# Optimization experiments

Hardware: AMD Instinct MI355X
Metric: run time of the kernel (lower is better)

## Reference

```python
import jax, jax.numpy as jnp
import numpy as np

N = 20000
E = 640000
D = 128      # node_dim
R = 32       # rbf_dim
H = 128      # radial_hidden_dim
CUTOFF = 5.0
RES_SCALE_INIT = 0.1
LN_EPS = 1e-5


def _init_linear(key, fan_in, fan_out):
    kw, kb = jax.random.split(key)
    bound = 1.0 / np.sqrt(fan_in)
    w = jax.random.uniform(kw, (fan_in, fan_out), minval=-bound, maxval=bound, dtype=jnp.float32)
    b = jax.random.uniform(kb, (fan_out,), minval=-bound, maxval=bound, dtype=jnp.float32)
    return w, b


def setup_inputs() -> dict:
    key = jax.random.key(0)
    ks = jax.random.split(key, 16)
    x = jax.random.normal(ks[0], (N, D), dtype=jnp.float32)
    edge_src = jax.random.randint(ks[1], (E,), 0, N)
    edge_dst = jax.random.randint(ks[2], (E,), 0, N)
    edge_sh = jax.random.normal(ks[3], (E, 16), dtype=jnp.float32)
    edge_rbf = jax.random.uniform(ks[4], (E, R), dtype=jnp.float32)
    edge_len = jax.random.uniform(ks[5], (E,), dtype=jnp.float32) * 8.0  # some edges beyond cutoff

    wm_w1, wm_b1 = _init_linear(ks[6], R, H)
    wm_w2, wm_b2 = _init_linear(ks[7], H, H)
    wm_w3, wm_b3 = _init_linear(ks[8], H, D)
    eg_w1, eg_b1 = _init_linear(ks[9], R, H)
    eg_w2, eg_b2 = _init_linear(ks[10], H, 1)
    mm_w1, mm_b1 = _init_linear(ks[11], D, H)
    mm_w2, mm_b2 = _init_linear(ks[12], H, D)
    sl_w, sl_b = _init_linear(ks[13], D, D)
    ul_w, ul_b = _init_linear(ks[14], D, D)

    return {
        "x": x, "edge_src": edge_src, "edge_dst": edge_dst,
        "edge_sh": edge_sh, "edge_rbf": edge_rbf, "edge_len": edge_len,
        "ln_g": jnp.ones((D,), jnp.float32), "ln_b": jnp.zeros((D,), jnp.float32),
        "wm_w1": wm_w1, "wm_b1": wm_b1, "wm_w2": wm_w2, "wm_b2": wm_b2,
        "wm_w3": wm_w3, "wm_b3": wm_b3,
        "eg_w1": eg_w1, "eg_b1": eg_b1, "eg_w2": eg_w2, "eg_b2": eg_b2,
        "mm_w1": mm_w1, "mm_b1": mm_b1, "mm_w2": mm_w2, "mm_b2": mm_b2,
        "sl_w": sl_w, "sl_b": sl_b, "ul_w": ul_w, "ul_b": ul_b,
        "res_scale": jnp.float32(RES_SCALE_INIT),
    }


def reference(x, edge_src, edge_dst, edge_sh, edge_rbf, edge_len,
              ln_g, ln_b,
              wm_w1, wm_b1, wm_w2, wm_b2, wm_w3, wm_b3,
              eg_w1, eg_b1, eg_w2, eg_b2,
              mm_w1, mm_b1, mm_w2, mm_b2,
              sl_w, sl_b, ul_w, ul_b, res_scale):
    # pre-LayerNorm
    mu = jnp.mean(x, axis=-1, keepdims=True)
    var = jnp.var(x, axis=-1, keepdims=True)
    x_norm = (x - mu) * jax.lax.rsqrt(var + LN_EPS) * ln_g + ln_b  # [N, D]

    # cosine cutoff * sigmoid edge gate -> [E, 1]
    r = edge_len / CUTOFF
    cut = 0.5 * (jnp.cos(jnp.pi * r) + 1.0) * (edge_len <= CUTOFF).astype(x.dtype)
    g = jax.nn.silu(edge_rbf @ eg_w1 + eg_b1)
    gate = jax.nn.sigmoid(g @ eg_w2 + eg_b2)  # [E, 1]
    edge_w = cut[:, None] * gate               # [E, 1]

    # radial weight MLP [E, D]
    h = jax.nn.silu(edge_rbf @ wm_w1 + wm_b1)
    h = jax.nn.silu(h @ wm_w2 + wm_b2)
    w_rad = h @ wm_w3 + wm_b3

    # gather, gate, scatter-add
    m = x_norm[edge_src] * w_rad * edge_w       # [E, D]
    agg = jax.ops.segment_sum(m, edge_dst, num_segments=N)          # [N, D]
    norm = jax.ops.segment_sum(edge_w, edge_dst, num_segments=N)    # [N, 1]
    agg = agg / jnp.maximum(norm, 1e-8)

    # message MLP + update
    a = jax.nn.silu(agg @ mm_w1 + mm_b1)
    agg2 = a @ mm_w2 + mm_b2
    out = (x_norm @ sl_w + sl_b) + (agg2 @ ul_w + ul_b)
    return x + res_scale * out
```

## Files before the change

kernel.cpp:

```cpp
#include <hip/hip_runtime.h>
#include <math.h>

#define N_NODES 20000
#define N_EDGES 640000
#define DD 128
#define RR 32
#define HH 128
#define PI_F 3.14159265358979323846f

#define NPACK 416
#define NLN   5000
#define NHIST 2500

typedef short bf16x8 __attribute__((ext_vector_type(8)));
typedef float f32x4 __attribute__((ext_vector_type(4)));
typedef __bf16 bf16x2_t __attribute__((ext_vector_type(2)));

__device__ __forceinline__ float silu_f(float x) {
    return x * __builtin_amdgcn_rcpf(1.0f + __expf(-x));
}
__device__ __forceinline__ float sigmoid_f(float x) {
    return __builtin_amdgcn_rcpf(1.0f + __expf(-x));
}
__device__ __forceinline__ unsigned short f2bf(float x) {
// ... 52 lines not shown
    } else if (blk < NPACK + NLN) {
        int wid = ((blk - NPACK) * 256 + threadIdx.x) >> 6;
        int lane = threadIdx.x & 63;
        if (wid >= N_NODES) return;
        const float* row = x + (size_t)wid * DD;
        float v0 = row[lane], v1 = row[lane + 64];
        float s = v0 + v1, sq = v0 * v0 + v1 * v1;
        #pragma unroll
        for (int o = 32; o > 0; o >>= 1) { s += __shfl_xor(s, o); sq += __shfl_xor(sq, o); }
        float mu = s * (1.0f / 128.0f);
        float var = sq * (1.0f / 128.0f) - mu * mu;
        float inv = rsqrtf(var + 1e-5f);
        float* orow = xn + (size_t)wid * DD;
        orow[lane]      = (v0 - mu) * inv * g[lane]      + b[lane];
        orow[lane + 64] = (v1 - mu) * inv * g[lane + 64] + b[lane + 64];
    } else {
        int e = (blk - NPACK - NLN) * 256 + threadIdx.x;
        if (e < N_EDGES && elen[e] <= 5.0f) atomicAdd(&cnt[edst[e]], 1);
    }
}

__global__ __launch_bounds__(1024) void scan_kernel(const int* __restrict__ cnt,
                                                    int* __restrict__ offs,
                                                    int* __restrict__ cursor) {
    __shared__ int part[1024];
    const int t = threadIdx.x;
    const int per = 20;
    const int base = t * per;
    int s = 0;
    for (int i = 0; i < per; ++i) {
        int idx = base + i;
        if (idx < N_NODES) s += cnt[idx];
    }
    part[t] = s;
    __syncthreads();
    for (int off = 1; off < 1024; off <<= 1) {
        int v = (t >= off) ? part[t - off] : 0;
        __syncthreads();
        part[t] += v;
        __syncthreads();
    }
    int run = part[t] - s;
    for (int i = 0; i < per; ++i) {
        int idx = base + i;
        if (idx < N_NODES) {
            offs[idx] = run;
            cursor[idx] = run;
            run += cnt[idx];
        }
    }
    if (t == 1023) offs[N_NODES] = part[1023];
}

__global__ __launch_bounds__(256) void fill_kernel(const int* __restrict__ edst,
                                                   const float* __restrict__ elen,
                                                   int* __restrict__ cursor,
                                                   int* __restrict__ perm) {
    int e = blockIdx.x * 256 + threadIdx.x;
    if (e >= N_EDGES) return;
    if (elen[e] <= 5.0f) {
        int pos = atomicAdd(&cursor[edst[e]], 1);
        perm[pos] = e;
    }
}

__global__ __launch_bounds__(256, 4) void edge_seg_kernel(
    const float* __restrict__ xn,
    const int* __restrict__ esrc, const int* __restrict__ edst,
    const float* __restrict__ rbf, const float* __restrict__ elen,
    const int* __restrict__ perm, const int* __restrict__ nlive_p,
    const unsigned short* __restrict__ wp_eg1, const unsigned short* __restrict__ wp_w1,
    const unsigned short* __restrict__ wp_w2,  const unsigned short* __restrict__ wp_w3,
    const float* __restrict__ eg_b1, const float* __restrict__ eg_w2,
    const float* __restrict__ eg_b2,
    const float* __restrict__ wm_b1, const float* __restrict__ wm_b2,
    const float* __restrict__ wm_b3,
    float* __restrict__ agg, float* __restrict__ nrm)
{
    __shared__ unsigned short act[4][32 * 136];
    __shared__ float ew_s[128];
    __shared__ int   dst_s[128];

    const int nlive = nlive_p[0];
    if (blockIdx.x * 128 >= nlive) return;

    const int tid  = threadIdx.x;
    const int w    = tid >> 6;
    const int lane = tid & 63;
    const int er   = lane & 15;
    const int kq   = lane >> 4;

    const int g0 = blockIdx.x * 128 + w * 32 + er;
    const int g1 = g0 + 16;
    const bool v0 = g0 < nlive, v1 = g1 < nlive;
    const int e0 = perm[v0 ? g0 : nlive - 1];
    const int e1 = perm[v1 ? g1 : nlive - 1];

    const float4* rp = (const float4*)(rbf + (size_t)e0 * RR + kq * 8);
    bf16x8 bfr0 = frag8(rp[0], rp[1]);
    const float4* rq = (const float4*)(rbf + (size_t)e1 * RR + kq * 8);
    bf16x8 bfr1 = frag8(rq[0], rq[1]);

    const int src0 = esrc[e0], dst0 = edst[e0];
    const int src1 = esrc[e1], dst1 = edst[e1];
    const float len0 = elen[e0], len1 = elen[e1];
    const float cut0 = v0 ? 0.5f * (__cosf(PI_F * len0 * 0.2f) + 1.0f) : 0.0f;
    const float cut1 = v1 ? 0.5f * (__cosf(PI_F * len1 * 0.2f) + 1.0f) : 0.0f;

    unsigned short* buf = &act[w][0];

    float pd0 = 0.0f, pd1 = 0.0f;
    #pragma unroll
    for (int t = 0; t < 8; ++t) {
        bf16x8 ag = *(const bf16x8*)(wp_eg1 + ((size_t)t * 64 + lane) * 8);
        bf16x8 a1 = *(const bf16x8*)(wp_w1  + ((size_t)t * 64 + lane) * 8);
        f32x4 z = {0.f, 0.f, 0.f, 0.f};
        f32x4 cg0 = __builtin_amdgcn_mfma_f32_16x16x32_bf16(ag, bfr0, z, 0, 0, 0);
        f32x4 cg1 = __builtin_amdgcn_mfma_f32_16x16x32_bf16(ag, bfr1, z, 0, 0, 0);
        f32x4 c10 = __builtin_amdgcn_mfma_f32_16x16x32_bf16(a1, bfr0, z, 0, 0, 0);
        f32x4 c11 = __builtin_amdgcn_mfma_f32_16x16x32_bf16(a1, bfr1, z, 0, 0, 0);
        float4 gb = *(const float4*)(eg_b1 + t * 16 + kq * 4);
        float4 w2 = *(const float4*)(eg_w2 + t * 16 + kq * 4);
        pd0 += silu_f(cg0[0]+gb.x)*w2.x + silu_f(cg0[1]+gb.y)*w2.y
             + silu_f(cg0[2]+gb.z)*w2.z + silu_f(cg0[3]+gb.w)*w2.w;
        pd1 += silu_f(cg1[0]+gb.x)*w2.x + silu_f(cg1[1]+gb.y)*w2.y
             + silu_f(cg1[2]+gb.z)*w2.z + silu_f(cg1[3]+gb.w)*w2.w;
        float4 b1 = *(const float4*)(wm_b1 + t * 16 + kq * 4);
        *(uint2*)(buf + er * 136 + t * 16 + kq * 4) =
            make_uint2(pk2(silu_f(c10[0]+b1.x), silu_f(c10[1]+b1.y)),
                       pk2(silu_f(c10[2]+b1.z), silu_f(c10[3]+b1.w)));
        *(uint2*)(buf + (16 + er) * 136 + t * 16 + kq * 4) =
            make_uint2(pk2(silu_f(c11[0]+b1.x), silu_f(c11[1]+b1.y)),
                       pk2(silu_f(c11[2]+b1.z), silu_f(c11[3]+b1.w)));
    }
    pd0 += __shfl_xor(pd0, 16); pd0 += __shfl_xor(pd0, 32);
    pd1 += __shfl_xor(pd1, 16); pd1 += __shfl_xor(pd1, 32);
    const float eb2 = eg_b2[0];
    const float ew0 = cut0 * sigmoid_f(pd0 + eb2);
    const float ew1 = cut1 * sigmoid_f(pd1 + eb2);
    if (lane < 16) {
        ew_s[w * 32 + er] = ew0;       dst_s[w * 32 + er] = dst0;
        ew_s[w * 32 + 16 + er] = ew1;  dst_s[w * 32 + 16 + er] = dst1;
    }

    bf16x8 h0[4], h1[4];
    #pragma unroll
    for (int s = 0; s < 4; ++s) {
        h0[s] = *(const bf16x8*)(buf + er * 136 + s * 32 + kq * 8);
        h1[s] = *(const bf16x8*)(buf + (16 + er) * 136 + s * 32 + kq * 8);
    }
    #pragma unroll
    for (int t = 0; t < 8; ++t) {
        f32x4 c0 = {0.f, 0.f, 0.f, 0.f};
        f32x4 c1 = {0.f, 0.f, 0.f, 0.f};
        #pragma unroll
        for (int s = 0; s < 4; ++s) {
            bf16x8 af = *(const bf16x8*)(wp_w2 + (((size_t)s * 8 + t) * 64 + lane) * 8);
            c0 = __builtin_amdgcn_mfma_f32_16x16x32_bf16(af, h0[s], c0, 0, 0, 0);
            c1 = __builtin_amdgcn_mfma_f32_16x16x32_bf16(af, h1[s], c1, 0, 0, 0);
        }
        float4 b2 = *(const float4*)(wm_b2 + t * 16 + kq * 4);
        *(uint2*)(buf + er * 136 + t * 16 + kq * 4) =
            make_uint2(pk2(silu_f(c0[0]+b2.x), silu_f(c0[1]+b2.y)),
                       pk2(silu_f(c0[2]+b2.z), silu_f(c0[3]+b2.w)));
        *(uint2*)(buf + (16 + er) * 136 + t * 16 + kq * 4) =
            make_uint2(pk2(silu_f(c1[0]+b2.x), silu_f(c1[1]+b2.y)),
                       pk2(silu_f(c1[2]+b2.z), silu_f(c1[3]+b2.w)));
    }

    #pragma unroll
    for (int s = 0; s < 4; ++s) {
        h0[s] = *(const bf16x8*)(buf + er * 136 + s * 32 + kq * 8);
        h1[s] = *(const bf16x8*)(buf + (16 + er) * 136 + s * 32 + kq * 8);
    }
    const float* xr0 = xn + (size_t)src0 * DD;
    const float* xr1 = xn + (size_t)src1 * DD;
    #pragma unroll
    for (int t = 0; t < 8; ++t) {
        f32x4 c0 = {0.f, 0.f, 0.f, 0.f};
        f32x4 c1 = {0.f, 0.f, 0.f, 0.f};
        #pragma unroll
        for (int s = 0; s < 4; ++s) {
            bf16x8 af = *(const bf16x8*)(wp_w3 + (((size_t)s * 8 + t) * 64 + lane) * 8);
            c0 = __builtin_amdgcn_mfma_f32_16x16x32_bf16(af, h0[s], c0, 0, 0, 0);
            c1 = __builtin_amdgcn_mfma_f32_16x16x32_bf16(af, h1[s], c1, 0, 0, 0);
        }
        float4 b3 = *(const float4*)(wm_b3 + t * 16 + kq * 4);
        float4 xv0 = *(const float4*)(xr0 + t * 16 + kq * 4);
        float4 xv1 = *(const float4*)(xr1 + t * 16 + kq * 4);
        *(uint2*)(buf + er * 136 + t * 16 + kq * 4) =
            make_uint2(pk2((c0[0]+b3.x)*xv0.x*ew0, (c0[1]+b3.y)*xv0.y*ew0),
                       pk2((c0[2]+b3.z)*xv0.z*ew0, (c0[3]+b3.w)*xv0.w*ew0));
        *(uint2*)(buf + (16 + er) * 136 + t * 16 + kq * 4) =
            make_uint2(pk2((c1[0]+b3.x)*xv1.x*ew1, (c1[1]+b3.y)*xv1.y*ew1),
                       pk2((c1[2]+b3.z)*xv1.z*ew1, (c1[3]+b3.w)*xv1.w*ew1));
    }

    {
        const int rb = w * 32;
        float run0 = 0.0f, run1 = 0.0f, ewrun = 0.0f;
        int cur = dst_s[rb];
        #pragma unroll 8
        for (int i = 0; i < 32; ++i) {
            const int d = dst_s[rb + i];
            if (d != cur) {
                atomicAdd(&agg[(size_t)cur * DD + 2 * lane], run0);
                atomicAdd(&agg[(size_t)cur * DD + 2 * lane + 1], run1);
                if (lane == 0) atomicAdd(&nrm[cur], ewrun);
                run0 = 0.0f; run1 = 0.0f; ewrun = 0.0f; cur = d;
            }
            unsigned pv = *(const unsigned*)(buf + i * 136 + 2 * lane);
            run0 += __uint_as_float(pv << 16);
            run1 += __uint_as_float(pv & 0xffff0000u);
            ewrun += ew_s[rb + i];
        }
        atomicAdd(&agg[(size_t)cur * DD + 2 * lane], run0);
        atomicAdd(&agg[(size_t)cur * DD + 2 * lane + 1], run1);
        if (lane == 0) atomicAdd(&nrm[cur], ewrun);
    }
}

__global__ __launch_bounds__(256) void node_kernel(
    const float* __restrict__ x, const float* __restrict__ xn,
    const float* __restrict__ agg, const float* __restrict__ nrm,
    const unsigned short* __restrict__ wp_mm1, const unsigned short* __restrict__ wp_mm2,
    const unsigned short* __restrict__ wp_sl,  const unsigned short* __restrict__ wp_ul,
    const float* __restrict__ mm_b1, const float* __restrict__ mm_b2,
    const float* __restrict__ sl_b, const float* __restrict__ ul_b,
    const float* __restrict__ res_scale, float* __restrict__ out)
{
    __shared__ unsigned short act[4][16 * 136];

    const int tid  = threadIdx.x;
    const int w    = tid >> 6;
    const int lane = tid & 63;
    const int er   = lane & 15;
    const int kq   = lane >> 4;

    const int n  = blockIdx.x * 64 + w * 16 + er;
    const bool valid = n < N_NODES;
    const int nc = valid ? n : N_NODES - 1;

    const float rs = __builtin_amdgcn_rcpf(fmaxf(nrm[nc], 1e-8f));
    const float rscl = res_scale[0];

    bf16x8 ba[4];
    #pragma unroll
    for (int s = 0; s < 4; ++s) {
        const float4* ap = (const float4*)(agg + (size_t)nc * DD + s * 32 + kq * 8);
        float4 a = ap[0], b = ap[1];
        a.x *= rs; a.y *= rs; a.z *= rs; a.w *= rs;
        b.x *= rs; b.y *= rs; b.z *= rs; b.w *= rs;
        ba[s] = frag8(a, b);
    }

    unsigned short* buf = &act[w][0];

    #pragma unroll
    for (int t = 0; t < 8; ++t) {
        f32x4 c = {0.f, 0.f, 0.f, 0.f};
        #pragma unroll
        for (int s = 0; s < 4; ++s) {
            bf16x8 af = *(const bf16x8*)(wp_mm1 + (((size_t)s * 8 + t) * 64 + lane) * 8);
            c = __builtin_amdgcn_mfma_f32_16x16x32_bf16(af, ba[s], c, 0, 0, 0);
        }
        float4 b1 = *(const float4*)(mm_b1 + t * 16 + kq * 4);
        *(uint2*)(buf + er * 136 + t * 16 + kq * 4) =
            make_uint2(pk2(silu_f(c[0]+b1.x), silu_f(c[1]+b1.y)),
                       pk2(silu_f(c[2]+b1.z), silu_f(c[3]+b1.w)));
    }

    bf16x8 bh[4];
    #pragma unroll
    for (int s = 0; s < 4; ++s)
        bh[s] = *(const bf16x8*)(buf + er * 136 + s * 32 + kq * 8);
    #pragma unroll
    for (int t = 0; t < 8; ++t) {
        f32x4 c = {0.f, 0.f, 0.f, 0.f};
        #pragma unroll
        for (int s = 0; s < 4; ++s) {
            bf16x8 af = *(const bf16x8*)(wp_mm2 + (((size_t)s * 8 + t) * 64 + lane) * 8);
            c = __builtin_amdgcn_mfma_f32_16x16x32_bf16(af, bh[s], c, 0, 0, 0);
        }
        float4 b2 = *(const float4*)(mm_b2 + t * 16 + kq * 4);
        *(uint2*)(buf + er * 136 + t * 16 + kq * 4) =
            make_uint2(pk2(c[0]+b2.x, c[1]+b2.y), pk2(c[2]+b2.z, c[3]+b2.w));
    }

    bf16x8 bg[4], bx[4];
    #pragma unroll
    for (int s = 0; s < 4; ++s) {
        bg[s] = *(const bf16x8*)(buf + er * 136 + s * 32 + kq * 8);
        const float4* xp = (const float4*)(xn + (size_t)nc * DD + s * 32 + kq * 8);
        bx[s] = frag8(xp[0], xp[1]);
    }

    #pragma unroll
    for (int t = 0; t < 8; ++t) {
        f32x4 c = {0.f, 0.f, 0.f, 0.f};
        #pragma unroll
        for (int s = 0; s < 4; ++s) {
            bf16x8 af = *(const bf16x8*)(wp_sl + (((size_t)s * 8 + t) * 64 + lane) * 8);
            c = __builtin_amdgcn_mfma_f32_16x16x32_bf16(af, bx[s], c, 0, 0, 0);
        }
        #pragma unroll
        for (int s = 0; s < 4; ++s) {
            bf16x8 af = *(const bf16x8*)(wp_ul + (((size_t)s * 8 + t) * 64 + lane) * 8);
            c = __builtin_amdgcn_mfma_f32_16x16x32_bf16(af, bg[s], c, 0, 0, 0);
        }
        if (valid) {
            float4 sb = *(const float4*)(sl_b + t * 16 + kq * 4);
            float4 ub = *(const float4*)(ul_b + t * 16 + kq * 4);
            float4 xv = *(const float4*)(x + (size_t)n * DD + t * 16 + kq * 4);
            float4 o;
            o.x = xv.x + rscl * (c[0] + sb.x + ub.x);
            o.y = xv.y + rscl * (c[1] + sb.y + ub.y);
            o.z = xv.z + rscl * (c[2] + sb.z + ub.z);
            o.w = xv.w + rscl * (c[3] + sb.w + ub.w);
            *(float4*)(out + (size_t)n * DD + t * 16 + kq * 4) = o;
        }
    }
}

extern "C" void kernel_launch(void* const* d_in, const int* in_sizes, int n_in,
                              void* d_out, int out_size, void* d_ws, size_t ws_size,
                              hipStream_t stream) {
    const float* x     = (const float*)d_in[0];
    const int*   esrc  = (const int*)d_in[1];
    const int*   edst  = (const int*)d_in[2];
    const float* rbf   = (const float*)d_in[4];
    const float* elen  = (const float*)d_in[5];
    const float* ln_g  = (const float*)d_in[6];
    const float* ln_b  = (const float*)d_in[7];
    const float* wm_w1 = (const float*)d_in[8];
    const float* wm_b1 = (const float*)d_in[9];
    const float* wm_w2 = (const float*)d_in[10];
    const float* wm_b2 = (const float*)d_in[11];
    const float* wm_w3 = (const float*)d_in[12];
    const float* wm_b3 = (const float*)d_in[13];
    const float* eg_w1 = (const float*)d_in[14];
    const float* eg_b1 = (const float*)d_in[15];
    const float* eg_w2 = (const float*)d_in[16];
    const float* eg_b2 = (const float*)d_in[17];
    const float* mm_w1 = (const float*)d_in[18];
    const float* mm_b1 = (const float*)d_in[19];
    const float* mm_w2 = (const float*)d_in[20];
    const float* mm_b2 = (const float*)d_in[21];
    const float* sl_w  = (const float*)d_in[22];
    const float* sl_b  = (const float*)d_in[23];
    const float* ul_w  = (const float*)d_in[24];
    const float* ul_b  = (const float*)d_in[25];
    const float* rscl  = (const float*)d_in[26];

    float* xn  = (float*)d_ws;
    float* agg = xn + (size_t)N_NODES * DD;
    float* nrm = agg + (size_t)N_NODES * DD;
    int*   cnt = (int*)(nrm + N_NODES);
    unsigned short* wp = (unsigned short*)(cnt + N_NODES);
    unsigned short* wp_eg1 = wp;
    unsigned short* wp_w1  = wp_eg1 + 4096;
    unsigned short* wp_w2  = wp_w1 + 4096;
    unsigned short* wp_w3  = wp_w2 + 16384;
    unsigned short* wp_mm1 = wp_w3 + 16384;
    unsigned short* wp_mm2 = wp_mm1 + 16384;
    unsigned short* wp_sl  = wp_mm2 + 16384;
    unsigned short* wp_ul  = wp_sl + 16384;
    int* offs   = (int*)(wp_ul + 16384);
    int* cursor = offs + N_NODES + 1;
    int* perm   = cursor + N_NODES;

    hipMemsetAsync(agg, 0, (size_t)(N_NODES * DD + 2 * N_NODES) * sizeof(float), stream);
    prep_kernel<<<NPACK + NLN + NHIST, 256, 0, stream>>>(
        eg_w1, wm_w1, wm_w2, wm_w3, mm_w1, mm_w2, sl_w, ul_w, wp,
        x, ln_g, ln_b, xn, edst, elen, cnt);
    scan_kernel<<<1, 1024, 0, stream>>>(cnt, offs, cursor);
    fill_kernel<<<N_EDGES / 256, 256, 0, stream>>>(edst, elen, cursor, perm);
    edge_seg_kernel<<<N_EDGES / 128, 256, 0, stream>>>(xn, esrc, edst, rbf, elen,
        perm, offs + N_NODES,
        wp_eg1, wp_w1, wp_w2, wp_w3,
        eg_b1, eg_w2, eg_b2, wm_b1, wm_b2, wm_b3, agg, nrm);
    node_kernel<<<(N_NODES + 63) / 64, 256, 0, stream>>>(x, xn, agg, nrm,
        wp_mm1, wp_mm2, wp_sl, wp_ul,
        mm_b1, mm_b2, sl_b, ul_b, rscl, (float*)d_out);
}
```

Baseline: 243.0 us.

## Process more edges and nodes per wave to reuse MFMA weight fragments

The edge kernel now handles 64 edges per wave (four 16-edge groups) instead of 32, so each weight fragment loaded from global memory feeds four MFMAs rather than two. Next-step weight fragments are prefetched into registers to overlap their loads with compute. The node kernel likewise processes 32 nodes per wave instead of 16. The cost is higher register and LDS use, so occupancy drops (launch bounds relaxed to 2 blocks per CU), and there are half as many blocks.

```diff
diff --git a/kernel.cpp b/kernel.cpp
--- a/kernel.cpp
+++ b/kernel.cpp
@@ -140,7 +140,7 @@
     }
 }
 
-__global__ __launch_bounds__(256, 4) void edge_seg_kernel(
+__global__ __launch_bounds__(256, 2) void edge_seg_kernel(
     const float* __restrict__ xn,
     const int* __restrict__ esrc, const int* __restrict__ edst,
     const float* __restrict__ rbf, const float* __restrict__ elen,
@@ -153,12 +153,12 @@
     const float* __restrict__ wm_b3,
     float* __restrict__ agg, float* __restrict__ nrm)
 {
-    __shared__ unsigned short act[4][32 * 136];
-    __shared__ float ew_s[128];
-    __shared__ int   dst_s[128];
+    __shared__ unsigned short act[4][64 * 136];
+    __shared__ float ew_s[256];
+    __shared__ int   dst_s[256];
 
     const int nlive = nlive_p[0];
-    if (blockIdx.x * 128 >= nlive) return;
+    if (blockIdx.x * 256 >= nlive) return;
 
     const int tid  = threadIdx.x;
     const int w    = tid >> 6;
@@ -166,118 +166,151 @@
     const int er   = lane & 15;
     const int kq   = lane >> 4;
 
-    const int g0 = blockIdx.x * 128 + w * 32 + er;
-    const int g1 = g0 + 16;
-    const bool v0 = g0 < nlive, v1 = g1 < nlive;
-    const int e0 = perm[v0 ? g0 : nlive - 1];
-    const int e1 = perm[v1 ? g1 : nlive - 1];
-
-    const float4* rp = (const float4*)(rbf + (size_t)e0 * RR + kq * 8);
-    bf16x8 bfr0 = frag8(rp[0], rp[1]);
-    const float4* rq = (const float4*)(rbf + (size_t)e1 * RR + kq * 8);
-    bf16x8 bfr1 = frag8(rq[0], rq[1]);
-
-    const int src0 = esrc[e0], dst0 = edst[e0];
-    const int src1 = esrc[e1], dst1 = edst[e1];
-    const float len0 = elen[e0], len1 = elen[e1];
-    const float cut0 = v0 ? 0.5f * (__cosf(PI_F * len0 * 0.2f) + 1.0f) : 0.0f;
-    const float cut1 = v1 ? 0.5f * (__cosf(PI_F * len1 * 0.2f) + 1.0f) : 0.0f;
+    const int gbase = blockIdx.x * 256 + w * 64 + er;
+    int eidx[4]; bool val[4];
+    #pragma unroll
+    for (int g = 0; g < 4; ++g) {
+        int gi = gbase + g * 16;
+        val[g] = gi < nlive;
+        eidx[g] = perm[val[g] ? gi : nlive - 1];
+    }
+
+    bf16x8 bfr[4];
+    int srcv[4];
+    float ew[4];
+    {
+        float cut[4]; int dstv[4];
+        #pragma unroll
+        for (int g = 0; g < 4; ++g) {
+            const float4* rp = (const float4*)(rbf + (size_t)eidx[g] * RR + kq * 8);
+            bfr[g] = frag8(rp[0], rp[1]);
+            srcv[g] = esrc[eidx[g]];
+            dstv[g] = edst[eidx[g]];
+            float len = elen[eidx[g]];
+            cut[g] = val[g] ? 0.5f * (__cosf(PI_F * len * 0.2f) + 1.0f) : 0.0f;
+        }
+
+        unsigned short* buf = &act[w][0];
+
+        float pd[4] = {0.f, 0.f, 0.f, 0.f};
+        bf16x8 agc = *(const bf16x8*)(wp_eg1 + (size_t)lane * 8);
+        bf16x8 a1c = *(const bf16x8*)(wp_w1  + (size_t)lane * 8);
+        #pragma unroll
+        for (int t = 0; t < 8; ++t) {
+            const int tn = (t + 1) & 7;
+            bf16x8 agn = *(const bf16x8*)(wp_eg1 + ((size_t)tn * 64 + lane) * 8);
+            bf16x8 a1n = *(const bf16x8*)(wp_w1  + ((size_t)tn * 64 + lane) * 8);
+            const f32x4 z = {0.f, 0.f, 0.f, 0.f};
+            float4 gb = *(const float4*)(eg_b1 + t * 16 + kq * 4);
+            float4 w2 = *(const float4*)(eg_w2 + t * 16 + kq * 4);
+            float4 b1 = *(const float4*)(wm_b1 + t * 16 + kq * 4);
+            #pragma unroll
+            for (int g = 0; g < 4; ++g) {
+                f32x4 cg = __builtin_amdgcn_mfma_f32_16x16x32_bf16(agc, bfr[g], z, 0, 0, 0);
+                f32x4 c1 = __builtin_amdgcn_mfma_f32_16x16x32_bf16(a1c, bfr[g], z, 0, 0, 0);
+                pd[g] += silu_f(cg[0]+gb.x)*w2.x + silu_f(cg[1]+gb.y)*w2.y
+                       + silu_f(cg[2]+gb.z)*w2.z + silu_f(cg[3]+gb.w)*w2.w;
+                *(uint2*)(buf + (g * 16 + er) * 136 + t * 16 + kq * 4) =
+                    make_uint2(pk2(silu_f(c1[0]+b1.x), silu_f(c1[1]+b1.y)),
+                               pk2(silu_f(c1[2]+b1.z), silu_f(c1[3]+b1.w)));
+            }
+            agc = agn; a1c = a1n;
+        }
+        const float eb2 = eg_b2[0];
+        #pragma unroll
+        for (int g = 0; g < 4; ++g) {
+            pd[g] += __shfl_xor(pd[g], 16);
+            pd[g] += __shfl_xor(pd[g], 32);
+            ew[g] = cut[g] * sigmoid_f(pd[g] + eb2);
+        }
+        if (lane < 16) {
+            #pragma unroll
+            for (int g = 0; g < 4; ++g) {
+                ew_s[w * 64 + g * 16 + er] = ew[g];
+                dst_s[w * 64 + g * 16 + er] = dstv[g];
+            }
+        }
+    }
 
     unsigned short* buf = &act[w][0];
 
-    float pd0 = 0.0f, pd1 = 0.0f;
-    #pragma unroll
-    for (int t = 0; t < 8; ++t) {
-        bf16x8 ag = *(const bf16x8*)(wp_eg1 + ((size_t)t * 64 + lane) * 8);
-        bf16x8 a1 = *(const bf16x8*)(wp_w1  + ((size_t)t * 64 + lane) * 8);
-        f32x4 z = {0.f, 0.f, 0.f, 0.f};
-        f32x4 cg0 = __builtin_amdgcn_mfma_f32_16x16x32_bf16(ag, bfr0, z, 0, 0, 0);
-        f32x4 cg1 = __builtin_amdgcn_mfma_f32_16x16x32_bf16(ag, bfr1, z, 0, 0, 0);
-        f32x4 c10 = __builtin_amdgcn_mfma_f32_16x16x32_bf16(a1, bfr0, z, 0, 0, 0);
-        f32x4 c11 = __builtin_amdgcn_mfma_f32_16x16x32_bf16(a1, bfr1, z, 0, 0, 0);
-        float4 gb = *(const float4*)(eg_b1 + t * 16 + kq * 4);
-        float4 w2 = *(const float4*)(eg_w2 + t * 16 + kq * 4);
-        pd0 += silu_f(cg0[0]+gb.x)*w2.x + silu_f(cg0[1]+gb.y)*w2.y
-             + silu_f(cg0[2]+gb.z)*w2.z + silu_f(cg0[3]+gb.w)*w2.w;
-        pd1 += silu_f(cg1[0]+gb.x)*w2.x + silu_f(cg1[1]+gb.y)*w2.y
-             + silu_f(cg1[2]+gb.z)*w2.z + silu_f(cg1[3]+gb.w)*w2.w;
-        float4 b1 = *(const float4*)(wm_b1 + t * 16 + kq * 4);
-        *(uint2*)(buf + er * 136 + t * 16 + kq * 4) =
-            make_uint2(pk2(silu_f(c10[0]+b1.x), silu_f(c10[1]+b1.y)),
-                       pk2(silu_f(c10[2]+b1.z), silu_f(c10[3]+b1.w)));
-        *(uint2*)(buf + (16 + er) * 136 + t * 16 + kq * 4) =
-            make_uint2(pk2(silu_f(c11[0]+b1.x), silu_f(c11[1]+b1.y)),
-                       pk2(silu_f(c11[2]+b1.z), silu_f(c11[3]+b1.w)));
-    }
-    pd0 += __shfl_xor(pd0, 16); pd0 += __shfl_xor(pd0, 32);
-    pd1 += __shfl_xor(pd1, 16); pd1 += __shfl_xor(pd1, 32);
-    const float eb2 = eg_b2[0];
-    const float ew0 = cut0 * sigmoid_f(pd0 + eb2);
-    const float ew1 = cut1 * sigmoid_f(pd1 + eb2);
-    if (lane < 16) {
-        ew_s[w * 32 + er] = ew0;       dst_s[w * 32 + er] = dst0;
-        ew_s[w * 32 + 16 + er] = ew1;  dst_s[w * 32 + 16 + er] = dst1;
-    }
-
-    bf16x8 h0[4], h1[4];
-    #pragma unroll
-    for (int s = 0; s < 4; ++s) {
-        h0[s] = *(const bf16x8*)(buf + er * 136 + s * 32 + kq * 8);
-        h1[s] = *(const bf16x8*)(buf + (16 + er) * 136 + s * 32 + kq * 8);
-    }
-    #pragma unroll
-    for (int t = 0; t < 8; ++t) {
-        f32x4 c0 = {0.f, 0.f, 0.f, 0.f};
-        f32x4 c1 = {0.f, 0.f, 0.f, 0.f};
-        #pragma unroll
-        for (int s = 0; s < 4; ++s) {
-            bf16x8 af = *(const bf16x8*)(wp_w2 + (((size_t)s * 8 + t) * 64 + lane) * 8);
-            c0 = __builtin_amdgcn_mfma_f32_16x16x32_bf16(af, h0[s], c0, 0, 0, 0);
-            c1 = __builtin_amdgcn_mfma_f32_16x16x32_bf16(af, h1[s], c1, 0, 0, 0);
-        }
-        float4 b2 = *(const float4*)(wm_b2 + t * 16 + kq * 4);
-        *(uint2*)(buf + er * 136 + t * 16 + kq * 4) =
-            make_uint2(pk2(silu_f(c0[0]+b2.x), silu_f(c0[1]+b2.y)),
-                       pk2(silu_f(c0[2]+b2.z), silu_f(c0[3]+b2.w)));
-        *(uint2*)(buf + (16 + er) * 136 + t * 16 + kq * 4) =
-            make_uint2(pk2(silu_f(c1[0]+b2.x), silu_f(c1[1]+b2.y)),
-                       pk2(silu_f(c1[2]+b2.z), silu_f(c1[3]+b2.w)));
-    }
-
-    #pragma unroll
-    for (int s = 0; s < 4; ++s) {
-        h0[s] = *(const bf16x8*)(buf + er * 136 + s * 32 + kq * 8);
-        h1[s] = *(const bf16x8*)(buf + (16 + er) * 136 + s * 32 + kq * 8);
-    }
-    const float* xr0 = xn + (size_t)src0 * DD;
-    const float* xr1 = xn + (size_t)src1 * DD;
-    #pragma unroll
-    for (int t = 0; t < 8; ++t) {
-        f32x4 c0 = {0.f, 0.f, 0.f, 0.f};
-        f32x4 c1 = {0.f, 0.f, 0.f, 0.f};
-        #pragma unroll
-        for (int s = 0; s < 4; ++s) {
-            bf16x8 af = *(const bf16x8*)(wp_w3 + (((size_t)s * 8 + t) * 64 + lane) * 8);
-            c0 = __builtin_amdgcn_mfma_f32_16x16x32_bf16(af, h0[s], c0, 0, 0, 0);
-            c1 = __builtin_amdgcn_mfma_f32_16x16x32_bf16(af, h1[s], c1, 0, 0, 0);
-        }
-        float4 b3 = *(const float4*)(wm_b3 + t * 16 + kq * 4);
-        float4 xv0 = *(const float4*)(xr0 + t * 16 + kq * 4);
-        float4 xv1 = *(const float4*)(xr1 + t * 16 + kq * 4);
-        *(uint2*)(buf + er * 136 + t * 16 + kq * 4) =
-            make_uint2(pk2((c0[0]+b3.x)*xv0.x*ew0, (c0[1]+b3.y)*xv0.y*ew0),
-                       pk2((c0[2]+b3.z)*xv0.z*ew0, (c0[3]+b3.w)*xv0.w*ew0));
-        *(uint2*)(buf + (16 + er) * 136 + t * 16 + kq * 4) =
-            make_uint2(pk2((c1[0]+b3.x)*xv1.x*ew1, (c1[1]+b3.y)*xv1.y*ew1),
-                       pk2((c1[2]+b3.z)*xv1.z*ew1, (c1[3]+b3.w)*xv1.w*ew1));
-    }
-
     {
-        const int rb = w * 32;
+        bf16x8 h[4][4];
+        #pragma unroll
+        for (int g = 0; g < 4; ++g)
+            #pragma unroll
+            for (int s = 0; s < 4; ++s)
+                h[g][s] = *(const bf16x8*)(buf + (g * 16 + er) * 136 + s * 32 + kq * 8);
+
+        bf16x8 afc[4];
+        #pragma unroll
+        for (int s = 0; s < 4; ++s)
+            afc[s] = *(const bf16x8*)(wp_w2 + (((size_t)s * 8 + 0) * 64 + lane) * 8);
+        #pragma unroll
+        for (int t = 0; t < 8; ++t) {
+            const int tn = (t + 1) & 7;
+            bf16x8 afn[4];
+            #pragma unroll
+            for (int s = 0; s < 4; ++s)
+                afn[s] = *(const bf16x8*)(wp_w2 + (((size_t)s * 8 + tn) * 64 + lane) * 8);
+            float4 b2 = *(const float4*)(wm_b2 + t * 16 + kq * 4);
+            #pragma unroll
+            for (int g = 0; g < 4; ++g) {
+                f32x4 c = {0.f, 0.f, 0.f, 0.f};
+                #pragma unroll
+                for (int s = 0; s < 4; ++s)
+                    c = __builtin_amdgcn_mfma_f32_16x16x32_bf16(afc[s], h[g][s], c, 0, 0, 0);
+                *(uint2*)(buf + (g * 16 + er) * 136 + t * 16 + kq * 4) =
+                    make_uint2(pk2(silu_f(c[0]+b2.x), silu_f(c[1]+b2.y)),
+                               pk2(silu_f(c[2]+b2.z), silu_f(c[3]+b2.w)));
+            }
+            #pragma unroll
+            for (int s = 0; s < 4; ++s) afc[s] = afn[s];
+        }
+    }
+
+    {
+        bf16x8 h[4][4];
+        #pragma unroll
+        for (int g = 0; g < 4; ++g)
+            #pragma unroll
+            for (int s = 0; s < 4; ++s)
+                h[g][s] = *(const bf16x8*)(buf + (g * 16 + er) * 136 + s * 32 + kq * 8);
+
+        bf16x8 afc[4];
+        #pragma unroll
+        for (int s = 0; s < 4; ++s)
+            afc[s] = *(const bf16x8*)(wp_w3 + (((size_t)s * 8 + 0) * 64 + lane) * 8);
+        #pragma unroll
+        for (int t = 0; t < 8; ++t) {
+            const int tn = (t + 1) & 7;
+            bf16x8 afn[4];
+            #pragma unroll
+            for (int s = 0; s < 4; ++s)
+                afn[s] = *(const bf16x8*)(wp_w3 + (((size_t)s * 8 + tn) * 64 + lane) * 8);
+            float4 b3 = *(const float4*)(wm_b3 + t * 16 + kq * 4);
+            #pragma unroll
+            for (int g = 0; g < 4; ++g) {
+                f32x4 c = {0.f, 0.f, 0.f, 0.f};
+                #pragma unroll
+                for (int s = 0; s < 4; ++s)
+                    c = __builtin_amdgcn_mfma_f32_16x16x32_bf16(afc[s], h[g][s], c, 0, 0, 0);
+                float4 xv = *(const float4*)(xn + (size_t)srcv[g] * DD + t * 16 + kq * 4);
+                *(uint2*)(buf + (g * 16 + er) * 136 + t * 16 + kq * 4) =
+                    make_uint2(pk2((c[0]+b3.x)*xv.x*ew[g], (c[1]+b3.y)*xv.y*ew[g]),
+                               pk2((c[2]+b3.z)*xv.z*ew[g], (c[3]+b3.w)*xv.w*ew[g]));
+            }
+            #pragma unroll
+            for (int s = 0; s < 4; ++s) afc[s] = afn[s];
+        }
+    }
+
+    {
+        const int rb = w * 64;
         float run0 = 0.0f, run1 = 0.0f, ewrun = 0.0f;
         int cur = dst_s[rb];
         #pragma unroll 8
-        for (int i = 0; i < 32; ++i) {
+        for (int i = 0; i < 64; ++i) {
             const int d = dst_s[rb + i];
             if (d != cur) {
                 atomicAdd(&agg[(size_t)cur * DD + 2 * lane], run0);
@@ -305,7 +338,7 @@
     const float* __restrict__ sl_b, const float* __restrict__ ul_b,
     const float* __restrict__ res_scale, float* __restrict__ out)
 {
-    __shared__ unsigned short act[4][16 * 136];
+    __shared__ unsigned short act[4][32 * 136];
 
     const int tid  = threadIdx.x;
     const int w    = tid >> 6;
@@ -313,87 +346,116 @@
     const int er   = lane & 15;
     const int kq   = lane >> 4;
 
-    const int n  = blockIdx.x * 64 + w * 16 + er;
-    const bool valid = n < N_NODES;
-    const int nc = valid ? n : N_NODES - 1;
-
-    const float rs = __builtin_amdgcn_rcpf(fmaxf(nrm[nc], 1e-8f));
+    const int n0 = blockIdx.x * 128 + w * 32 + er;
+    const int n1 = n0 + 16;
+    const bool val0 = n0 < N_NODES, val1 = n1 < N_NODES;
+    const int nc0 = val0 ? n0 : N_NODES - 1;
+    const int nc1 = val1 ? n1 : N_NODES - 1;
+
+    const float rs0 = __builtin_amdgcn_rcpf(fmaxf(nrm[nc0], 1e-8f));
+    const float rs1 = __builtin_amdgcn_rcpf(fmaxf(nrm[nc1], 1e-8f));
     const float rscl = res_scale[0];
 
-    bf16x8 ba[4];
+    bf16x8 ba0[4], ba1[4];
     #pragma unroll
     for (int s = 0; s < 4; ++s) {
-        const float4* ap = (const float4*)(agg + (size_t)nc * DD + s * 32 + kq * 8);
+        const float4* ap = (const float4*)(agg + (size_t)nc0 * DD + s * 32 + kq * 8);
         float4 a = ap[0], b = ap[1];
-        a.x *= rs; a.y *= rs; a.z *= rs; a.w *= rs;
-        b.x *= rs; b.y *= rs; b.z *= rs; b.w *= rs;
-        ba[s] = frag8(a, b);
+        a.x*=rs0; a.y*=rs0; a.z*=rs0; a.w*=rs0; b.x*=rs0; b.y*=rs0; b.z*=rs0; b.w*=rs0;
+        ba0[s] = frag8(a, b);
+        const float4* aq = (const float4*)(agg + (size_t)nc1 * DD + s * 32 + kq * 8);
+        float4 c = aq[0], d = aq[1];
+        c.x*=rs1; c.y*=rs1; c.z*=rs1; c.w*=rs1; d.x*=rs1; d.y*=rs1; d.z*=rs1; d.w*=rs1;
+        ba1[s] = frag8(c, d);
     }
 
     unsigned short* buf = &act[w][0];
 
     #pragma unroll
     for (int t = 0; t < 8; ++t) {
-        f32x4 c = {0.f, 0.f, 0.f, 0.f};
+        f32x4 c0 = {0.f,0.f,0.f,0.f}, c1 = {0.f,0.f,0.f,0.f};
         #pragma unroll
         for (int s = 0; s < 4; ++s) {
             bf16x8 af = *(const bf16x8*)(wp_mm1 + (((size_t)s * 8 + t) * 64 + lane) * 8);
-            c = __builtin_amdgcn_mfma_f32_16x16x32_bf16(af, ba[s], c, 0, 0, 0);
+            c0 = __builtin_amdgcn_mfma_f32_16x16x32_bf16(af, ba0[s], c0, 0, 0, 0);
+            c1 = __builtin_amdgcn_mfma_f32_16x16x32_bf16(af, ba1[s], c1, 0, 0, 0);
         }
         float4 b1 = *(const float4*)(mm_b1 + t * 16 + kq * 4);
         *(uint2*)(buf + er * 136 + t * 16 + kq * 4) =
-            make_uint2(pk2(silu_f(c[0]+b1.x), silu_f(c[1]+b1.y)),
-                       pk2(silu_f(c[2]+b1.z), silu_f(c[3]+b1.w)));
-    }
-
-    bf16x8 bh[4];
-    #pragma unroll
-    for (int s = 0; s < 4; ++s)
-        bh[s] = *(const bf16x8*)(buf + er * 136 + s * 32 + kq * 8);
+            make_uint2(pk2(silu_f(c0[0]+b1.x), silu_f(c0[1]+b1.y)),
+                       pk2(silu_f(c0[2]+b1.z), silu_f(c0[3]+b1.w)));
+        *(uint2*)(buf + (16 + er) * 136 + t * 16 + kq * 4) =
+            make_uint2(pk2(silu_f(c1[0]+b1.x), silu_f(c1[1]+b1.y)),
+                       pk2(silu_f(c1[2]+b1.z), silu_f(c1[3]+b1.w)));
+    }
+
+    bf16x8 bh0[4], bh1[4];
+    #pragma unroll
+    for (int s = 0; s < 4; ++s) {
+        bh0[s] = *(const bf16x8*)(buf + er * 136 + s * 32 + kq * 8);
+        bh1[s] = *(const bf16x8*)(buf + (16 + er) * 136 + s * 32 + kq * 8);
+    }
     #pragma unroll
     for (int t = 0; t < 8; ++t) {
-        f32x4 c = {0.f, 0.f, 0.f, 0.f};
+        f32x4 c0 = {0.f,0.f,0.f,0.f}, c1 = {0.f,0.f,0.f,0.f};
         #pragma unroll
         for (int s = 0; s < 4; ++s) {
             bf16x8 af = *(const bf16x8*)(wp_mm2 + (((size_t)s * 8 + t) * 64 + lane) * 8);
-            c = __builtin_amdgcn_mfma_f32_16x16x32_bf16(af, bh[s], c, 0, 0, 0);
+            c0 = __builtin_amdgcn_mfma_f32_16x16x32_bf16(af, bh0[s], c0, 0, 0, 0);
+            c1 = __builtin_amdgcn_mfma_f32_16x16x32_bf16(af, bh1[s], c1, 0, 0, 0);
         }
         float4 b2 = *(const float4*)(mm_b2 + t * 16 + kq * 4);
         *(uint2*)(buf + er * 136 + t * 16 + kq * 4) =
-            make_uint2(pk2(c[0]+b2.x, c[1]+b2.y), pk2(c[2]+b2.z, c[3]+b2.w));
-    }
-
-    bf16x8 bg[4], bx[4];
+            make_uint2(pk2(c0[0]+b2.x, c0[1]+b2.y), pk2(c0[2]+b2.z, c0[3]+b2.w));
+        *(uint2*)(buf + (16 + er) * 136 + t * 16 + kq * 4) =
+            make_uint2(pk2(c1[0]+b2.x, c1[1]+b2.y), pk2(c1[2]+b2.z, c1[3]+b2.w));
+    }
+
+    bf16x8 bg0[4], bg1[4], bx0[4], bx1[4];
     #pragma unroll
     for (int s = 0; s < 4; ++s) {
-        bg[s] = *(const bf16x8*)(buf + er * 136 + s * 32 + kq * 8);
-        const float4* xp = (const float4*)(xn + (size_t)nc * DD + s * 32 + kq * 8);
-        bx[s] = frag8(xp[0], xp[1]);
+        bg0[s] = *(const bf16x8*)(buf + er * 136 + s * 32 + kq * 8);
+        bg1[s] = *(const bf16x8*)(buf + (16 + er) * 136 + s * 32 + kq * 8);
+        const float4* xp = (const float4*)(xn + (size_t)nc0 * DD + s * 32 + kq * 8);
+        bx0[s] = frag8(xp[0], xp[1]);
+        const float4* xq = (const float4*)(xn + (size_t)nc1 * DD + s * 32 + kq * 8);
+        bx1[s] = frag8(xq[0], xq[1]);
     }
 
     #pragma unroll
     for (int t = 0; t < 8; ++t) {
-        f32x4 c = {0.f, 0.f, 0.f, 0.f};
+        f32x4 c0 = {0.f,0.f,0.f,0.f}, c1 = {0.f,0.f,0.f,0.f};
         #pragma unroll
         for (int s = 0; s < 4; ++s) {
             bf16x8 af = *(const bf16x8*)(wp_sl + (((size_t)s * 8 + t) * 64 + lane) * 8);
-            c = __builtin_amdgcn_mfma_f32_16x16x32_bf16(af, bx[s], c, 0, 0, 0);
+            c0 = __builtin_amdgcn_mfma_f32_16x16x32_bf16(af, bx0[s], c0, 0, 0, 0);
+            c1 = __builtin_amdgcn_mfma_f32_16x16x32_bf16(af, bx1[s], c1, 0, 0, 0);
         }
         #pragma unroll
         for (int s = 0; s < 4; ++s) {
             bf16x8 af = *(const bf16x8*)(wp_ul + (((size_t)s * 8 + t) * 64 + lane) * 8);
-            c = __builtin_amdgcn_mfma_f32_16x16x32_bf16(af, bg[s], c, 0, 0, 0);
-        }
-        if (valid) {
-            float4 sb = *(const float4*)(sl_b + t * 16 + kq * 4);
-            float4 ub = *(const float4*)(ul_b + t * 16 + kq * 4);
-            float4 xv = *(const float4*)(x + (size_t)n * DD + t * 16 + kq * 4);
+            c0 = __builtin_amdgcn_mfma_f32_16x16x32_bf16(af, bg0[s], c0, 0, 0, 0);
+            c1 = __builtin_amdgcn_mfma_f32_16x16x32_bf16(af, bg1[s], c1, 0, 0, 0);
+        }
+        float4 sb = *(const float4*)(sl_b + t * 16 + kq * 4);
+        float4 ub = *(const float4*)(ul_b + t * 16 + kq * 4);
+        if (val0) {
+            float4 xv = *(const float4*)(x + (size_t)n0 * DD + t * 16 + kq * 4);
             float4 o;
-            o.x = xv.x + rscl * (c[0] + sb.x + ub.x);
-            o.y = xv.y + rscl * (c[1] + sb.y + ub.y);
-            o.z = xv.z + rscl * (c[2] + sb.z + ub.z);
-            o.w = xv.w + rscl * (c[3] + sb.w + ub.w);
-            *(float4*)(out + (size_t)n * DD + t * 16 + kq * 4) = o;
+            o.x = xv.x + rscl * (c0[0] + sb.x + ub.x);
+            o.y = xv.y + rscl * (c0[1] + sb.y + ub.y);
+            o.z = xv.z + rscl * (c0[2] + sb.z + ub.z);
+            o.w = xv.w + rscl * (c0[3] + sb.w + ub.w);
+            *(float4*)(out + (size_t)n0 * DD + t * 16 + kq * 4) = o;
+        }
+        if (val1) {
+            float4 xv = *(const float4*)(x + (size_t)n1 * DD + t * 16 + kq * 4);
+            float4 o;
+            o.x = xv.x + rscl * (c1[0] + sb.x + ub.x);
+            o.y = xv.y + rscl * (c1[1] + sb.y + ub.y);
+            o.z = xv.z + rscl * (c1[2] + sb.z + ub.z);
+            o.w = xv.w + rscl * (c1[3] + sb.w + ub.w);
+            *(float4*)(out + (size_t)n1 * DD + t * 16 + kq * 4) = o;
         }
     }
 }
@@ -451,11 +513,11 @@
         x, ln_g, ln_b, xn, edst, elen, cnt);
     scan_kernel<<<1, 1024, 0, stream>>>(cnt, offs, cursor);
     fill_kernel<<<N_EDGES / 256, 256, 0, stream>>>(edst, elen, cursor, perm);
-    edge_seg_kernel<<<N_EDGES / 128, 256, 0, stream>>>(xn, esrc, edst, rbf, elen,
+    edge_seg_kernel<<<N_EDGES / 256, 256, 0, stream>>>(xn, esrc, edst, rbf, elen,
         perm, offs + N_NODES,
         wp_eg1, wp_w1, wp_w2, wp_w3,
         eg_b1, eg_w2, eg_b2, wm_b1, wm_b2, wm_b3, agg, nrm);
-    node_kernel<<<(N_NODES + 63) / 64, 256, 0, stream>>>(x, xn, agg, nrm,
+    node_kernel<<<(N_NODES + 127) / 128, 256, 0, stream>>>(x, xn, agg, nrm,
         wp_mm1, wp_mm2, wp_sl, wp_ul,
         mm_b1, mm_b2, sl_b, ul_b, rscl, (float*)d_out);
 }
```

After: 228.2 us. 6.1% less time.

## Pack sorted edge records with src/dst/cutoff; process 32 nodes per wave in node kernel

Applied to the files above, without the earlier changes.

The fill kernel now writes a 16-byte record per live edge holding the edge id, source, destination and precomputed cosine cutoff. The edge kernel then reads one contiguous record instead of gathering esrc, edst and elen scattered through the perm indirection. Separately, the node kernel now handles two 16-node tiles per wave so each loaded weight fragment feeds two MFMAs, halving weight reloads and the grid size. The cost is a larger permutation buffer, more fill-kernel writes and higher register pressure in the node kernel.

```diff
diff --git a/kernel.cpp b/kernel.cpp
--- a/kernel.cpp
+++ b/kernel.cpp
@@ -128,23 +128,31 @@
     if (t == 1023) offs[N_NODES] = part[1023];
 }
 
-__global__ __launch_bounds__(256) void fill_kernel(const int* __restrict__ edst,
+__global__ __launch_bounds__(256) void fill_kernel(const int* __restrict__ esrc,
+                                                   const int* __restrict__ edst,
                                                    const float* __restrict__ elen,
                                                    int* __restrict__ cursor,
-                                                   int* __restrict__ perm) {
+                                                   int4* __restrict__ erec) {
     int e = blockIdx.x * 256 + threadIdx.x;
     if (e >= N_EDGES) return;
-    if (elen[e] <= 5.0f) {
-        int pos = atomicAdd(&cursor[edst[e]], 1);
-        perm[pos] = e;
+    float len = elen[e];
+    if (len <= 5.0f) {
+        int d = edst[e];
+        int pos = atomicAdd(&cursor[d], 1);
+        float cut = 0.5f * (__cosf(PI_F * len * 0.2f) + 1.0f);
+        int4 rec;
+        rec.x = e;
+        rec.y = esrc[e];
+        rec.z = d;
+        rec.w = __float_as_int(cut);
+        erec[pos] = rec;
     }
 }
 
 __global__ __launch_bounds__(256, 4) void edge_seg_kernel(
     const float* __restrict__ xn,
-    const int* __restrict__ esrc, const int* __restrict__ edst,
-    const float* __restrict__ rbf, const float* __restrict__ elen,
-    const int* __restrict__ perm, const int* __restrict__ nlive_p,
+    const float* __restrict__ rbf,
+    const int4* __restrict__ erec, const int* __restrict__ nlive_p,
     const unsigned short* __restrict__ wp_eg1, const unsigned short* __restrict__ wp_w1,
     const unsigned short* __restrict__ wp_w2,  const unsigned short* __restrict__ wp_w3,
     const float* __restrict__ eg_b1, const float* __restrict__ eg_w2,
@@ -169,20 +177,19 @@
     const int g0 = blockIdx.x * 128 + w * 32 + er;
     const int g1 = g0 + 16;
     const bool v0 = g0 < nlive, v1 = g1 < nlive;
-    const int e0 = perm[v0 ? g0 : nlive - 1];
-    const int e1 = perm[v1 ? g1 : nlive - 1];
+    const int4 r0 = erec[v0 ? g0 : nlive - 1];
+    const int4 r1 = erec[v1 ? g1 : nlive - 1];
+
+    const int e0 = r0.x, src0 = r0.y, dst0 = r0.z;
+    const int e1 = r1.x, src1 = r1.y, dst1 = r1.z;
+    const float cut0 = v0 ? __int_as_float(r0.w) : 0.0f;
+    const float cut1 = v1 ? __int_as_float(r1.w) : 0.0f;
 
     const float4* rp = (const float4*)(rbf + (size_t)e0 * RR + kq * 8);
     bf16x8 bfr0 = frag8(rp[0], rp[1]);
     const float4* rq = (const float4*)(rbf + (size_t)e1 * RR + kq * 8);
     bf16x8 bfr1 = frag8(rq[0], rq[1]);
 
-    const int src0 = esrc[e0], dst0 = edst[e0];
-    const int src1 = esrc[e1], dst1 = edst[e1];
-    const float len0 = elen[e0], len1 = elen[e1];
-    const float cut0 = v0 ? 0.5f * (__cosf(PI_F * len0 * 0.2f) + 1.0f) : 0.0f;
-    const float cut1 = v1 ? 0.5f * (__cosf(PI_F * len1 * 0.2f) + 1.0f) : 0.0f;
-
     unsigned short* buf = &act[w][0];
 
     float pd0 = 0.0f, pd1 = 0.0f;
@@ -190,7 +197,7 @@
     for (int t = 0; t < 8; ++t) {
         bf16x8 ag = *(const bf16x8*)(wp_eg1 + ((size_t)t * 64 + lane) * 8);
         bf16x8 a1 = *(const bf16x8*)(wp_w1  + ((size_t)t * 64 + lane) * 8);
-        f32x4 z = {0.f, 0.f, 0.f, 0.f};
+        const f32x4 z = {0.f, 0.f, 0.f, 0.f};
         f32x4 cg0 = __builtin_amdgcn_mfma_f32_16x16x32_bf16(ag, bfr0, z, 0, 0, 0);
         f32x4 cg1 = __builtin_amdgcn_mfma_f32_16x16x32_bf16(ag, bfr1, z, 0, 0, 0);
         f32x4 c10 = __builtin_amdgcn_mfma_f32_16x16x32_bf16(a1, bfr0, z, 0, 0, 0);
@@ -305,7 +312,7 @@
     const float* __restrict__ sl_b, const float* __restrict__ ul_b,
     const float* __restrict__ res_scale, float* __restrict__ out)
 {
-    __shared__ unsigned short act[4][16 * 136];
+    __shared__ unsigned short act[4][32 * 136];
 
     const int tid  = threadIdx.x;
     const int w    = tid >> 6;
@@ -313,87 +320,116 @@
     const int er   = lane & 15;
     const int kq   = lane >> 4;
 
-    const int n  = blockIdx.x * 64 + w * 16 + er;
-    const bool valid = n < N_NODES;
-    const int nc = valid ? n : N_NODES - 1;
-
-    const float rs = __builtin_amdgcn_rcpf(fmaxf(nrm[nc], 1e-8f));
+    const int n0 = blockIdx.x * 128 + w * 32 + er;
+    const int n1 = n0 + 16;
+    const bool val0 = n0 < N_NODES, val1 = n1 < N_NODES;
+    const int nc0 = val0 ? n0 : N_NODES - 1;
+    const int nc1 = val1 ? n1 : N_NODES - 1;
+
+    const float rs0 = __builtin_amdgcn_rcpf(fmaxf(nrm[nc0], 1e-8f));
+    const float rs1 = __builtin_amdgcn_rcpf(fmaxf(nrm[nc1], 1e-8f));
     const float rscl = res_scale[0];
 
-    bf16x8 ba[4];
+    bf16x8 ba0[4], ba1[4];
     #pragma unroll
     for (int s = 0; s < 4; ++s) {
-        const float4* ap = (const float4*)(agg + (size_t)nc * DD + s * 32 + kq * 8);
+        const float4* ap = (const float4*)(agg + (size_t)nc0 * DD + s * 32 + kq * 8);
         float4 a = ap[0], b = ap[1];
-        a.x *= rs; a.y *= rs; a.z *= rs; a.w *= rs;
-        b.x *= rs; b.y *= rs; b.z *= rs; b.w *= rs;
-        ba[s] = frag8(a, b);
+        a.x*=rs0; a.y*=rs0; a.z*=rs0; a.w*=rs0; b.x*=rs0; b.y*=rs0; b.z*=rs0; b.w*=rs0;
+        ba0[s] = frag8(a, b);
+        const float4* aq = (const float4*)(agg + (size_t)nc1 * DD + s * 32 + kq * 8);
+        float4 c = aq[0], d = aq[1];
+        c.x*=rs1; c.y*=rs1; c.z*=rs1; c.w*=rs1; d.x*=rs1; d.y*=rs1; d.z*=rs1; d.w*=rs1;
+        ba1[s] = frag8(c, d);
     }
 
     unsigned short* buf = &act[w][0];
 
     #pragma unroll
     for (int t = 0; t < 8; ++t) {
-        f32x4 c = {0.f, 0.f, 0.f, 0.f};
+        f32x4 c0 = {0.f,0.f,0.f,0.f}, c1 = {0.f,0.f,0.f,0.f};
         #pragma unroll
         for (int s = 0; s < 4; ++s) {
             bf16x8 af = *(const bf16x8*)(wp_mm1 + (((size_t)s * 8 + t) * 64 + lane) * 8);
-            c = __builtin_amdgcn_mfma_f32_16x16x32_bf16(af, ba[s], c, 0, 0, 0);
+            c0 = __builtin_amdgcn_mfma_f32_16x16x32_bf16(af, ba0[s], c0, 0, 0, 0);
+            c1 = __builtin_amdgcn_mfma_f32_16x16x32_bf16(af, ba1[s], c1, 0, 0, 0);
         }
         float4 b1 = *(const float4*)(mm_b1 + t * 16 + kq * 4);
         *(uint2*)(buf + er * 136 + t * 16 + kq * 4) =
-            make_uint2(pk2(silu_f(c[0]+b1.x), silu_f(c[1]+b1.y)),
-                       pk2(silu_f(c[2]+b1.z), silu_f(c[3]+b1.w)));
-    }
-
-    bf16x8 bh[4];
-    #pragma unroll
-    for (int s = 0; s < 4; ++s)
-        bh[s] = *(const bf16x8*)(buf + er * 136 + s * 32 + kq * 8);
-    #pragma unroll
-    for (int t = 0; t < 8; ++t) {
-        f32x4 c = {0.f, 0.f, 0.f, 0.f};
+            make_uint2(pk2(silu_f(c0[0]+b1.x), silu_f(c0[1]+b1.y)),
+                       pk2(silu_f(c0[2]+b1.z), silu_f(c0[3]+b1.w)));
+        *(uint2*)(buf + (16 + er) * 136 + t * 16 + kq * 4) =
+            make_uint2(pk2(silu_f(c1[0]+b1.x), silu_f(c1[1]+b1.y)),
+                       pk2(silu_f(c1[2]+b1.z), silu_f(c1[3]+b1.w)));
+    }
+
+    bf16x8 bh0[4], bh1[4];
+    #pragma unroll
+    for (int s = 0; s < 4; ++s) {
+        bh0[s] = *(const bf16x8*)(buf + er * 136 + s * 32 + kq * 8);
+        bh1[s] = *(const bf16x8*)(buf + (16 + er) * 136 + s * 32 + kq * 8);
+    }
+    #pragma unroll
+    for (int t = 0; t < 8; ++t) {
+        f32x4 c0 = {0.f,0.f,0.f,0.f}, c1 = {0.f,0.f,0.f,0.f};
         #pragma unroll
         for (int s = 0; s < 4; ++s) {
             bf16x8 af = *(const bf16x8*)(wp_mm2 + (((size_t)s * 8 + t) * 64 + lane) * 8);
-            c = __builtin_amdgcn_mfma_f32_16x16x32_bf16(af, bh[s], c, 0, 0, 0);
+            c0 = __builtin_amdgcn_mfma_f32_16x16x32_bf16(af, bh0[s], c0, 0, 0, 0);
+            c1 = __builtin_amdgcn_mfma_f32_16x16x32_bf16(af, bh1[s], c1, 0, 0, 0);
         }
         float4 b2 = *(const float4*)(mm_b2 + t * 16 + kq * 4);
         *(uint2*)(buf + er * 136 + t * 16 + kq * 4) =
-            make_uint2(pk2(c[0]+b2.x, c[1]+b2.y), pk2(c[2]+b2.z, c[3]+b2.w));
-    }
-
-    bf16x8 bg[4], bx[4];
+            make_uint2(pk2(c0[0]+b2.x, c0[1]+b2.y), pk2(c0[2]+b2.z, c0[3]+b2.w));
+        *(uint2*)(buf + (16 + er) * 136 + t * 16 + kq * 4) =
+            make_uint2(pk2(c1[0]+b2.x, c1[1]+b2.y), pk2(c1[2]+b2.z, c1[3]+b2.w));
+    }
+
+    bf16x8 bg0[4], bg1[4], bx0[4], bx1[4];
     #pragma unroll
     for (int s = 0; s < 4; ++s) {
-        bg[s] = *(const bf16x8*)(buf + er * 136 + s * 32 + kq * 8);
-        const float4* xp = (const float4*)(xn + (size_t)nc * DD + s * 32 + kq * 8);
-        bx[s] = frag8(xp[0], xp[1]);
-    }
-
-    #pragma unroll
-    for (int t = 0; t < 8; ++t) {
-        f32x4 c = {0.f, 0.f, 0.f, 0.f};
+        bg0[s] = *(const bf16x8*)(buf + er * 136 + s * 32 + kq * 8);
+        bg1[s] = *(const bf16x8*)(buf + (16 + er) * 136 + s * 32 + kq * 8);
+        const float4* xp = (const float4*)(xn + (size_t)nc0 * DD + s * 32 + kq * 8);
+        bx0[s] = frag8(xp[0], xp[1]);
+        const float4* xq = (const float4*)(xn + (size_t)nc1 * DD + s * 32 + kq * 8);
+        bx1[s] = frag8(xq[0], xq[1]);
+    }
+
+    #pragma unroll
+    for (int t = 0; t < 8; ++t) {
+        f32x4 c0 = {0.f,0.f,0.f,0.f}, c1 = {0.f,0.f,0.f,0.f};
         #pragma unroll
         for (int s = 0; s < 4; ++s) {
             bf16x8 af = *(const bf16x8*)(wp_sl + (((size_t)s * 8 + t) * 64 + lane) * 8);
-            c = __builtin_amdgcn_mfma_f32_16x16x32_bf16(af, bx[s], c, 0, 0, 0);
+            c0 = __builtin_amdgcn_mfma_f32_16x16x32_bf16(af, bx0[s], c0, 0, 0, 0);
+            c1 = __builtin_amdgcn_mfma_f32_16x16x32_bf16(af, bx1[s], c1, 0, 0, 0);
         }
         #pragma unroll
         for (int s = 0; s < 4; ++s) {
             bf16x8 af = *(const bf16x8*)(wp_ul + (((size_t)s * 8 + t) * 64 + lane) * 8);
-            c = __builtin_amdgcn_mfma_f32_16x16x32_bf16(af, bg[s], c, 0, 0, 0);
-        }
-        if (valid) {
-            float4 sb = *(const float4*)(sl_b + t * 16 + kq * 4);
-            float4 ub = *(const float4*)(ul_b + t * 16 + kq * 4);
-            float4 xv = *(const float4*)(x + (size_t)n * DD + t * 16 + kq * 4);
+            c0 = __builtin_amdgcn_mfma_f32_16x16x32_bf16(af, bg0[s], c0, 0, 0, 0);
+            c1 = __builtin_amdgcn_mfma_f32_16x16x32_bf16(af, bg1[s], c1, 0, 0, 0);
+        }
+        float4 sb = *(const float4*)(sl_b + t * 16 + kq * 4);
+        float4 ub = *(const float4*)(ul_b + t * 16 + kq * 4);
+        if (val0) {
+            float4 xv = *(const float4*)(x + (size_t)n0 * DD + t * 16 + kq * 4);
             float4 o;
-            o.x = xv.x + rscl * (c[0] + sb.x + ub.x);
-            o.y = xv.y + rscl * (c[1] + sb.y + ub.y);
-            o.z = xv.z + rscl * (c[2] + sb.z + ub.z);
-            o.w = xv.w + rscl * (c[3] + sb.w + ub.w);
-            *(float4*)(out + (size_t)n * DD + t * 16 + kq * 4) = o;
+            o.x = xv.x + rscl * (c0[0] + sb.x + ub.x);
+            o.y = xv.y + rscl * (c0[1] + sb.y + ub.y);
+            o.z = xv.z + rscl * (c0[2] + sb.z + ub.z);
+            o.w = xv.w + rscl * (c0[3] + sb.w + ub.w);
+            *(float4*)(out + (size_t)n0 * DD + t * 16 + kq * 4) = o;
+        }
+        if (val1) {
+            float4 xv = *(const float4*)(x + (size_t)n1 * DD + t * 16 + kq * 4);
+            float4 o;
+            o.x = xv.x + rscl * (c1[0] + sb.x + ub.x);
+            o.y = xv.y + rscl * (c1[1] + sb.y + ub.y);
+            o.z = xv.z + rscl * (c1[2] + sb.z + ub.z);
+            o.w = xv.w + rscl * (c1[3] + sb.w + ub.w);
+            *(float4*)(out + (size_t)n1 * DD + t * 16 + kq * 4) = o;
         }
     }
 }
@@ -443,19 +479,18 @@
     unsigned short* wp_ul  = wp_sl + 16384;
     int* offs   = (int*)(wp_ul + 16384);
     int* cursor = offs + N_NODES + 1;
-    int* perm   = cursor + N_NODES;
+    int4* erec  = (int4*)(((size_t)(cursor + N_NODES) + 15) & ~(size_t)15);
 
     hipMemsetAsync(agg, 0, (size_t)(N_NODES * DD + 2 * N_NODES) * sizeof(float), stream);
     prep_kernel<<<NPACK + NLN + NHIST, 256, 0, stream>>>(
         eg_w1, wm_w1, wm_w2, wm_w3, mm_w1, mm_w2, sl_w, ul_w, wp,
         x, ln_g, ln_b, xn, edst, elen, cnt);
     scan_kernel<<<1, 1024, 0, stream>>>(cnt, offs, cursor);
-    fill_kernel<<<N_EDGES / 256, 256, 0, stream>>>(edst, elen, cursor, perm);
-    edge_seg_kernel<<<N_EDGES / 128, 256, 0, stream>>>(xn, esrc, edst, rbf, elen,
-        perm, offs + N_NODES,
+    fill_kernel<<<N_EDGES / 256, 256, 0, stream>>>(esrc, edst, elen, cursor, erec);
+    edge_seg_kernel<<<N_EDGES / 128, 256, 0, stream>>>(xn, rbf, erec, offs + N_NODES,
         wp_eg1, wp_w1, wp_w2, wp_w3,
         eg_b1, eg_w2, eg_b2, wm_b1, wm_b2, wm_b3, agg, nrm);
-    node_kernel<<<(N_NODES + 63) / 64, 256, 0, stream>>>(x, xn, agg, nrm,
+    node_kernel<<<(N_NODES + 127) / 128, 256, 0, stream>>>(x, xn, agg, nrm,
         wp_mm1, wp_mm2, wp_sl, wp_ul,
         mm_b1, mm_b2, sl_b, ul_b, rscl, (float*)d_out);
 }
```

Measured after the change: 239.1 us. Within noise of the previous version (-1.6%).
